# Optimization experiments

Hardware: AMD Instinct MI355X
Metric: run time of the kernel (lower is better)

The kernel has to match this reference:

```python
import jax, jax.numpy as jnp
import numpy as np

B, SX, SY, H = 4, 512, 512, 128


def setup_inputs() -> dict:
    key = jax.random.key(0)
    k1, k2, k3, k4, k5 = jax.random.split(key, 5)
    x = jax.random.normal(k1, (B, SX, 2 * H), dtype=jnp.float32)
    y = jax.random.normal(k2, (B, SY, 2 * H), dtype=jnp.float32)
    # nn.Linear(in, out, bias=False) weight has shape (out, in)
    s = 1.0 / np.sqrt(2 * H)
    Wc1 = jax.random.uniform(k3, (H, 2 * H), minval=-s, maxval=s, dtype=jnp.float32)
    Wc2 = jax.random.uniform(k4, (H, 2 * H), minval=-s, maxval=s, dtype=jnp.float32)
    sv = 1.0 / np.sqrt(H)
    vc = jax.random.uniform(k5, (1, H), minval=-sv, maxval=sv, dtype=jnp.float32)
    return {"x": x, "y": y, "Wc1": Wc1, "Wc2": Wc2, "vc": vc}


def reference(x, y, Wc1, Wc2, vc):
    # s1: (B, Sx, H), s2: (B, Sy, H)
    s1 = jnp.einsum('bsd,hd->bsh', x, Wc1)
    s2 = jnp.einsum('btd,hd->bth', y, Wc2)
    # broadcast tanh-MLP score: (B, Sy, Sx, H) -> (B, Sy, Sx)
    sjt = jnp.einsum('btsh,h->bts', jnp.tanh(s1[:, None, :, :] + s2[:, :, None, :]), vc[0])
    ait = jax.nn.softmax(sjt, axis=2)  # softmax over Sx
    qtc = jnp.einsum('bts,bsd->btd', ait, x)  # (B, Sy, 2H)
    return qtc
```

## Files before the change

kernel.cpp:

```cpp
#include <hip/hip_runtime.h>


#define NB 4
#define SEQ 512
#define HDIM 128
#define DDIM 256

static constexpr float TWO_LOG2E = 2.8853900817779268f;
static constexpr float LOG2E     = 1.4426950408889634f;

__global__ __launch_bounds__(256) void wtrans_kernel(
    const float* __restrict__ W1, const float* __restrict__ W2,
    float* __restrict__ Wt1, float* __restrict__ Wt2)
{
    __shared__ float sT[32 * 132];
    const int blk = blockIdx.x;
    const int which = blk >> 3;
    const int s = blk & 7;
    const float* W  = which ? W2 : W1;
    float*       Wt = which ? Wt2 : Wt1;
    const int tid = threadIdx.x;

    #pragma unroll
    for (int i = 0; i < 4; ++i) {
        const int idx = i * 256 + tid;
        const int h = idx >> 3, k4 = idx & 7;
        const float4 v = ((const float4*)W)[h * 64 + s * 8 + k4];
        sT[(k4 * 4 + 0) * 132 + h] = v.x;
        sT[(k4 * 4 + 1) * 132 + h] = v.y;
        sT[(k4 * 4 + 2) * 132 + h] = v.z;
        sT[(k4 * 4 + 3) * 132 + h] = v.w;
    }
    __syncthreads();
    #pragma unroll
    for (int i = 0; i < 4; ++i) {
        const int idx = i * 256 + tid;
        const int kl = idx >> 5, hq = idx & 31;
        float4 o;
        o.x = sT[kl * 132 + 4 * hq + 0];
        o.y = sT[kl * 132 + 4 * hq + 1];
        o.z = sT[kl * 132 + 4 * hq + 2];
        o.w = sT[kl * 132 + 4 * hq + 3];
        ((float4*)Wt)[(s * 32 + kl) * 32 + hq] = o;
    }
}

__global__ __launch_bounds__(256) void proj_kernel(
    const float* __restrict__ x, const float* __restrict__ y,
    const float* __restrict__ Wt1, const float* __restrict__ Wt2,
    float* __restrict__ e1sw, float* __restrict__ e2)
{
    __shared__ float As[2048];
    __shared__ float sPr[8192];
    const int tid = threadIdx.x;
    const int gr0 = blockIdx.x * 8;

    const float* in; const float* Wt; int srow;
    if (gr0 < 2048) { in = x; Wt = Wt1; srow = gr0; }
    else            { in = y; Wt = Wt2; srow = gr0 - 2048; }

    #pragma unroll
    for (int j = 0; j < 2; ++j) {
        const int idx = tid + j * 256;
        const int r = idx >> 6, kk = idx & 63;
        *(float4*)&As[idx * 4] =
            *(const float4*)&in[(srow + r) * 256 + kk * 4];
    }
    __syncthreads();

    const int hq = tid & 31;
    const int ks = tid >> 5;
    const float4* Wt4 = (const float4*)Wt;

    float4 acc4[8];
    #pragma unroll
    for (int r = 0; r < 8; ++r) acc4[r] = make_float4(0.f, 0.f, 0.f, 0.f);

    #pragma unroll
    for (int u = 0; u < 8; ++u) {
        const int kof = ks * 32 + u * 4;
        const float4 w0 = Wt4[(kof + 0) * 32 + hq];
        const float4 w1 = Wt4[(kof + 1) * 32 + hq];
        const float4 w2 = Wt4[(kof + 2) * 32 + hq];
        const float4 w3 = Wt4[(kof + 3) * 32 + hq];
        #pragma unroll
        for (int r = 0; r < 8; ++r) {
            const float4 a = *(const float4*)&As[r * 256 + kof];
            acc4[r].x = fmaf(a.w,w3.x, fmaf(a.z,w2.x, fmaf(a.y,w1.x, fmaf(a.x,w0.x, acc4[r].x))));
            acc4[r].y = fmaf(a.w,w3.y, fmaf(a.z,w2.y, fmaf(a.y,w1.y, fmaf(a.x,w0.y, acc4[r].y))));
            acc4[r].z = fmaf(a.w,w3.z, fmaf(a.z,w2.z, fmaf(a.y,w1.z, fmaf(a.x,w0.z, acc4[r].z))));
            acc4[r].w = fmaf(a.w,w3.w, fmaf(a.z,w2.w, fmaf(a.y,w1.w, fmaf(a.x,w0.w, acc4[r].w))));
        }
    }
    #pragma unroll
    for (int r = 0; r < 8; ++r)
        *(float4*)&sPr[ks * 1024 + r * 128 + hq * 4] = acc4[r];
    __syncthreads();
    {
        const int r = tid >> 5, h4 = tid & 31;
        float4 s = make_float4(0.f, 0.f, 0.f, 0.f);
        #pragma unroll
        for (int k2 = 0; k2 < 8; ++k2) {
            const float4 p = *(const float4*)&sPr[k2 * 1024 + r * 128 + h4 * 4];
            s.x += p.x; s.y += p.y; s.z += p.z; s.w += p.w;
        }
        float4 o;
        o.x = __builtin_amdgcn_exp2f(s.x * TWO_LOG2E);
        o.y = __builtin_amdgcn_exp2f(s.y * TWO_LOG2E);
        o.z = __builtin_amdgcn_exp2f(s.z * TWO_LOG2E);
        o.w = __builtin_amdgcn_exp2f(s.w * TWO_LOG2E);
        const int gr = gr0 + r;
        if (gr < 2048) {
            const int b = gr >> 9, ss = gr & 511;
            const int c = ss >> 6, sl = ss & 63;
            ((float4*)e1sw)[((b * 8 + c) * 32 + h4) * 64 + (sl ^ h4)] = o;
        } else {
            ((float4*)e2)[(gr - 2048) * 32 + h4] = o;
        }
    }
}

__global__ __launch_bounds__(1024) void score_kernel(
    const float* __restrict__ e1sw, const float* __restrict__ e2g,
    const float* __restrict__ vc,  float* __restrict__ P)
{
    __shared__ float sPartC[2][2][16 * 256];
    __shared__ float sScore[4 * 512];

    const int tid  = threadIdx.x;
    const int b    = blockIdx.x >> 7;
    const int t0   = (blockIdx.x & 127) * 4;
    const int w    = tid >> 6;
    const int lane = tid & 63;
    const int wu   = __builtin_amdgcn_readfirstlane(w);
    const int hg   = wu;

    float4 vcs[2];
    float4 e2s[4][2];
    #pragma unroll
    for (int j = 0; j < 2; ++j)
        vcs[j] = *(const float4*)&vc[(hg * 2 + j) * 4];
    #pragma unroll
    for (int t = 0; t < 4; ++t)
        #pragma unroll
        for (int j = 0; j < 2; ++j)
            e2s[t][j] = *(const float4*)&e2g[(b * SEQ + t0 + t) * HDIM + (hg * 2 + j) * 4];

    const float4* e1c = (const float4*)e1sw + b * 16384;

    const int off0 = (hg * 2 + 0) * 64 + (lane ^ (hg * 2 + 0));
    const int off1 = (hg * 2 + 1) * 64 + (lane ^ (hg * 2 + 1));

    float4 e1v0 = e1c[off0];
    float4 e1v1 = e1c[off1];

    for (int c = 0; c < 8; ++c) {
        float4 e1n0 = e1v0, e1n1 = e1v1;
        if (c < 7) {
            const float4* nx = e1c + (c + 1) * 2048;
            e1n0 = nx[off0];
            e1n1 = nx[off1];
        }
        float acc0 = 0.f, acc1 = 0.f, acc2 = 0.f, acc3 = 0.f;
        #pragma unroll
        for (int j = 0; j < 2; ++j) {
            const float4 e1 = j ? e1v1 : e1v0;
            const float4 vv = vcs[j];
            #pragma unroll
            for (int t = 0; t < 4; ++t) {
                const float4 e2 = e2s[t][j];
                const float f1 = fmaf(e1.x, e2.x, 1.f);
                const float f2 = fmaf(e1.y, e2.y, 1.f);
                const float f3 = fmaf(e1.z, e2.z, 1.f);
                const float f4 = fmaf(e1.w, e2.w, 1.f);
                const float f12 = f1 * f2, f34 = f3 * f4;
                const float n12 = fmaf(vv.x, f2, vv.y * f1);
                const float n34 = fmaf(vv.z, f4, vv.w * f3);
                const float num = fmaf(n12, f34, n34 * f12);
                const float r = fmaf(num, __builtin_amdgcn_rcpf(f12 * f34),
                                     (t == 0) ? acc0 : (t == 1) ? acc1 : (t == 2) ? acc2 : acc3);
                if      (t == 0) acc0 = r;
                else if (t == 1) acc1 = r;
                else if (t == 2) acc2 = r;
                else             acc3 = r;
            }
        }
        float* pb = &sPartC[(c >> 1) & 1][c & 1][0] + wu * 256 + lane;
        pb[0 * 64] = acc0;
        pb[1 * 64] = acc1;
        pb[2 * 64] = acc2;
        pb[3 * 64] = acc3;
        if (c & 1) {
            __syncthreads();
            if (tid < 512) {
                const int ch = tid >> 8;
                const int t  = (tid >> 6) & 3, s = tid & 63;
                const float* pc = &sPartC[(c >> 1) & 1][ch][0] + t * 64 + s;
                float r = 0.f;
                #pragma unroll
                for (int ww = 0; ww < 16; ++ww) r += pc[ww * 256];
                sScore[t * 512 + (c - 1 + ch) * 64 + s] = -2.f * r;
            }
        }
        e1v0 = e1n0;
        e1v1 = e1n1;
    }
    __syncthreads();

    if (w < 4) {
        float v[8];
        float m = -1e30f;
        #pragma unroll
        for (int j = 0; j < 8; ++j) {
            v[j] = sScore[w * 512 + lane + j * 64];
            m = fmaxf(m, v[j]);
        }
        #pragma unroll
        for (int off = 32; off; off >>= 1) m = fmaxf(m, __shfl_xor(m, off));
        float sum = 0.f;
        #pragma unroll
        for (int j = 0; j < 8; ++j) {
            v[j] = __builtin_amdgcn_exp2f((v[j] - m) * LOG2E);
            sum += v[j];
        }
        #pragma unroll
        for (int off = 32; off; off >>= 1) sum += __shfl_xor(sum, off);
        const float inv = __builtin_amdgcn_rcpf(sum);
        float* Prow = &P[(b * SEQ + t0 + w) * SEQ];
        #pragma unroll
        for (int j = 0; j < 8; ++j)
            Prow[lane + j * 64] = v[j] * inv;
    }
}

__global__ __launch_bounds__(1024) void pax_kernel(
    const float* __restrict__ P, const float* __restrict__ x,
    float* __restrict__ out)
{
    __shared__ float sP[SEQ * 8];
    __shared__ float sRed[8 * 8 * DDIM];
    const int tid = threadIdx.x;
    const int b   = blockIdx.x >> 6;
    const int t0  = (blockIdx.x & 63) * 8;
    const int w    = tid >> 6;
    const int lane = tid & 63;

    {
        const int t = tid >> 7, c4 = tid & 127;
        const float4 p = *(const float4*)&P[(b * SEQ + t0 + t) * SEQ + c4 * 4];
        sP[(c4 * 4 + 0) * 8 + t] = p.x;
        sP[(c4 * 4 + 1) * 8 + t] = p.y;
        sP[(c4 * 4 + 2) * 8 + t] = p.z;
        sP[(c4 * 4 + 3) * 8 + t] = p.w;
    }
    __syncthreads();

    const float4* x4 = (const float4*)x;
    float4 acc[8];
    #pragma unroll
    for (int t = 0; t < 8; ++t) acc[t] = make_float4(0.f, 0.f, 0.f, 0.f);

    #pragma unroll 4
    for (int si = 0; si < 32; ++si) {
        const int s = w * 32 + si;
        const float4 xv  = x4[(b * SEQ + s) * 64 + lane];
        const float4 p03 = *(const float4*)&sP[s * 8];
        const float4 p47 = *(const float4*)&sP[s * 8 + 4];
        acc[0].x = fmaf(p03.x, xv.x, acc[0].x); acc[0].y = fmaf(p03.x, xv.y, acc[0].y);
        acc[0].z = fmaf(p03.x, xv.z, acc[0].z); acc[0].w = fmaf(p03.x, xv.w, acc[0].w);
        acc[1].x = fmaf(p03.y, xv.x, acc[1].x); acc[1].y = fmaf(p03.y, xv.y, acc[1].y);
        acc[1].z = fmaf(p03.y, xv.z, acc[1].z); acc[1].w = fmaf(p03.y, xv.w, acc[1].w);
        acc[2].x = fmaf(p03.z, xv.x, acc[2].x); acc[2].y = fmaf(p03.z, xv.y, acc[2].y);
        acc[2].z = fmaf(p03.z, xv.z, acc[2].z); acc[2].w = fmaf(p03.z, xv.w, acc[2].w);
        acc[3].x = fmaf(p03.w, xv.x, acc[3].x); acc[3].y = fmaf(p03.w, xv.y, acc[3].y);
        acc[3].z = fmaf(p03.w, xv.z, acc[3].z); acc[3].w = fmaf(p03.w, xv.w, acc[3].w);
        acc[4].x = fmaf(p47.x, xv.x, acc[4].x); acc[4].y = fmaf(p47.x, xv.y, acc[4].y);
        acc[4].z = fmaf(p47.x, xv.z, acc[4].z); acc[4].w = fmaf(p47.x, xv.w, acc[4].w);
        acc[5].x = fmaf(p47.y, xv.x, acc[5].x); acc[5].y = fmaf(p47.y, xv.y, acc[5].y);
        acc[5].z = fmaf(p47.y, xv.z, acc[5].z); acc[5].w = fmaf(p47.y, xv.w, acc[5].w);
        acc[6].x = fmaf(p47.z, xv.x, acc[6].x); acc[6].y = fmaf(p47.z, xv.y, acc[6].y);
        acc[6].z = fmaf(p47.z, xv.z, acc[6].z); acc[6].w = fmaf(p47.z, xv.w, acc[6].w);
        acc[7].x = fmaf(p47.w, xv.x, acc[7].x); acc[7].y = fmaf(p47.w, xv.y, acc[7].y);
        acc[7].z = fmaf(p47.w, xv.z, acc[7].z); acc[7].w = fmaf(p47.w, xv.w, acc[7].w);
    }

    float4* sRed4 = (float4*)sRed;
    if (w < 8) {
        #pragma unroll
        for (int t = 0; t < 8; ++t)
            sRed4[w * 512 + t * 64 + lane] = acc[t];
    }
    __syncthreads();
    if (w >= 8) {
        #pragma unroll
        for (int t = 0; t < 8; ++t) {
            float4 r = sRed4[(w - 8) * 512 + t * 64 + lane];
            r.x += acc[t].x; r.y += acc[t].y; r.z += acc[t].z; r.w += acc[t].w;
            sRed4[(w - 8) * 512 + t * 64 + lane] = r;
        }
    }
    __syncthreads();
    #pragma unroll
    for (int j = 0; j < 2; ++j) {
        const int i = tid + j * 1024;
        const int t = i >> 8, d = i & 255;
        float r = 0.f;
        #pragma unroll
        for (int q = 0; q < 8; ++q) r += sRed[q * 2048 + t * 256 + d];
        out[(b * SEQ + t0 + t) * DDIM + d] = r;
    }
}

extern "C" void kernel_launch(void* const* d_in, const int* in_sizes, int n_in,
                              void* d_out, int out_size, void* d_ws, size_t ws_size,
                              hipStream_t stream) {
    const float* x   = (const float*)d_in[0];
    const float* y   = (const float*)d_in[1];
    const float* W1  = (const float*)d_in[2];
    const float* W2  = (const float*)d_in[3];
    const float* vc  = (const float*)d_in[4];
    float* outp = (float*)d_out;

    float* ws  = (float*)d_ws;
    float* e1  = ws;
    float* e2  = ws + NB * SEQ * HDIM;
    float* P   = ws + 2 * NB * SEQ * HDIM;
    float* Wt1 = P + NB * SEQ * SEQ;
    float* Wt2 = Wt1 + HDIM * DDIM;

    hipLaunchKernelGGL(wtrans_kernel, dim3(16),  dim3(256),  0, stream,
                       W1, W2, Wt1, Wt2);
    hipLaunchKernelGGL(proj_kernel,   dim3(512), dim3(256),  0, stream,
                       x, y, Wt1, Wt2, e1, e2);
    hipLaunchKernelGGL(score_kernel,  dim3(512), dim3(1024), 0, stream,
                       e1, e2, vc, P);
    hipLaunchKernelGGL(pax_kernel,    dim3(256), dim3(1024), 0, stream,
                       P, x, outp);
}
```

Before: 97.98 us.

## Fuse score/softmax kernel with P·x kernel, keeping probabilities in LDS

Merges the score+softmax kernel and the probability-times-x kernel into one launch. Each block now handles 8 query rows instead of 4, and the softmax result goes straight into shared memory instead of a global P buffer. This removes the global write and read of the 4x512x512 probability matrix and one kernel launch. In exchange the grid is halved to 256 blocks, register pressure rises from doubled e2 and accumulator state, and the score phase now syncs every chunk rather than every other chunk.

```diff
diff --git a/kernel.cpp b/kernel.cpp
--- a/kernel.cpp
+++ b/kernel.cpp
@@ -120,28 +120,28 @@
     }
 }
 
-__global__ __launch_bounds__(1024) void score_kernel(
+__global__ __launch_bounds__(1024) void score_pax_kernel(
     const float* __restrict__ e1sw, const float* __restrict__ e2g,
-    const float* __restrict__ vc,  float* __restrict__ P)
+    const float* __restrict__ vc,  const float* __restrict__ x,
+    float* __restrict__ out)
 {
-    __shared__ float sPartC[2][2][16 * 256];
-    __shared__ float sScore[4 * 512];
+    __shared__ float sBig[16384];
 
     const int tid  = threadIdx.x;
-    const int b    = blockIdx.x >> 7;
-    const int t0   = (blockIdx.x & 127) * 4;
+    const int b    = blockIdx.x >> 6;
+    const int t0   = (blockIdx.x & 63) * 8;
     const int w    = tid >> 6;
     const int lane = tid & 63;
     const int wu   = __builtin_amdgcn_readfirstlane(w);
     const int hg   = wu;
 
     float4 vcs[2];
-    float4 e2s[4][2];
+    float4 e2s[8][2];
     #pragma unroll
     for (int j = 0; j < 2; ++j)
         vcs[j] = *(const float4*)&vc[(hg * 2 + j) * 4];
     #pragma unroll
-    for (int t = 0; t < 4; ++t)
+    for (int t = 0; t < 8; ++t)
         #pragma unroll
         for (int j = 0; j < 2; ++j)
             e2s[t][j] = *(const float4*)&e2g[(b * SEQ + t0 + t) * HDIM + (hg * 2 + j) * 4];
@@ -153,6 +153,8 @@
 
     float4 e1v0 = e1c[off0];
     float4 e1v1 = e1c[off1];
+
+    float v[8];
 
     for (int c = 0; c < 8; ++c) {
         float4 e1n0 = e1v0, e1n1 = e1v1;
@@ -161,13 +163,15 @@
             e1n0 = nx[off0];
             e1n1 = nx[off1];
         }
-        float acc0 = 0.f, acc1 = 0.f, acc2 = 0.f, acc3 = 0.f;
+        float acc[8];
+        #pragma unroll
+        for (int t = 0; t < 8; ++t) acc[t] = 0.f;
         #pragma unroll
         for (int j = 0; j < 2; ++j) {
             const float4 e1 = j ? e1v1 : e1v0;
             const float4 vv = vcs[j];
             #pragma unroll
-            for (int t = 0; t < 4; ++t) {
+            for (int t = 0; t < 8; ++t) {
                 const float4 e2 = e2s[t][j];
                 const float f1 = fmaf(e1.x, e2.x, 1.f);
                 const float f2 = fmaf(e1.y, e2.y, 1.f);
@@ -177,44 +181,30 @@
                 const float n12 = fmaf(vv.x, f2, vv.y * f1);
                 const float n34 = fmaf(vv.z, f4, vv.w * f3);
                 const float num = fmaf(n12, f34, n34 * f12);
-                const float r = fmaf(num, __builtin_amdgcn_rcpf(f12 * f34),
-                                     (t == 0) ? acc0 : (t == 1) ? acc1 : (t == 2) ? acc2 : acc3);
-                if      (t == 0) acc0 = r;
-                else if (t == 1) acc1 = r;
-                else if (t == 2) acc2 = r;
-                else             acc3 = r;
+                acc[t] = fmaf(num, __builtin_amdgcn_rcpf(f12 * f34), acc[t]);
             }
         }
-        float* pb = &sPartC[(c >> 1) & 1][c & 1][0] + wu * 256 + lane;
-        pb[0 * 64] = acc0;
-        pb[1 * 64] = acc1;
-        pb[2 * 64] = acc2;
-        pb[3 * 64] = acc3;
-        if (c & 1) {
-            __syncthreads();
-            if (tid < 512) {
-                const int ch = tid >> 8;
-                const int t  = (tid >> 6) & 3, s = tid & 63;
-                const float* pc = &sPartC[(c >> 1) & 1][ch][0] + t * 64 + s;
-                float r = 0.f;
-                #pragma unroll
-                for (int ww = 0; ww < 16; ++ww) r += pc[ww * 256];
-                sScore[t * 512 + (c - 1 + ch) * 64 + s] = -2.f * r;
-            }
+        float* pb = sBig + (c & 1) * 8192 + wu * 512 + lane;
+        #pragma unroll
+        for (int t = 0; t < 8; ++t) pb[t * 64] = acc[t];
+        __syncthreads();
+        if (tid < 512) {
+            const int t = tid >> 6, s = tid & 63;
+            const float* pc = sBig + (c & 1) * 8192 + t * 64 + s;
+            float r = 0.f;
+            #pragma unroll
+            for (int ww = 0; ww < 16; ++ww) r += pc[ww * 512];
+            v[c] = -2.f * r;
         }
         e1v0 = e1n0;
         e1v1 = e1n1;
     }
-    __syncthreads();
-
-    if (w < 4) {
-        float v[8];
+
+    if (tid < 512) {
+        const int t = w;
         float m = -1e30f;
         #pragma unroll
-        for (int j = 0; j < 8; ++j) {
-            v[j] = sScore[w * 512 + lane + j * 64];
-            m = fmaxf(m, v[j]);
-        }
+        for (int j = 0; j < 8; ++j) m = fmaxf(m, v[j]);
         #pragma unroll
         for (int off = 32; off; off >>= 1) m = fmaxf(m, __shfl_xor(m, off));
         float sum = 0.f;
@@ -226,32 +216,9 @@
         #pragma unroll
         for (int off = 32; off; off >>= 1) sum += __shfl_xor(sum, off);
         const float inv = __builtin_amdgcn_rcpf(sum);
-        float* Prow = &P[(b * SEQ + t0 + w) * SEQ];
         #pragma unroll
         for (int j = 0; j < 8; ++j)
-            Prow[lane + j * 64] = v[j] * inv;
-    }
-}
-
-__global__ __launch_bounds__(1024) void pax_kernel(
-    const float* __restrict__ P, const float* __restrict__ x,
-    float* __restrict__ out)
-{
-    __shared__ float sP[SEQ * 8];
-    __shared__ float sRed[8 * 8 * DDIM];
-    const int tid = threadIdx.x;
-    const int b   = blockIdx.x >> 6;
-    const int t0  = (blockIdx.x & 63) * 8;
-    const int w    = tid >> 6;
-    const int lane = tid & 63;
-
-    {
-        const int t = tid >> 7, c4 = tid & 127;
-        const float4 p = *(const float4*)&P[(b * SEQ + t0 + t) * SEQ + c4 * 4];
-        sP[(c4 * 4 + 0) * 8 + t] = p.x;
-        sP[(c4 * 4 + 1) * 8 + t] = p.y;
-        sP[(c4 * 4 + 2) * 8 + t] = p.z;
-        sP[(c4 * 4 + 3) * 8 + t] = p.w;
+            sBig[(j * 64 + lane) * 8 + t] = v[j] * inv;
     }
     __syncthreads();
 
@@ -264,8 +231,8 @@
     for (int si = 0; si < 32; ++si) {
         const int s = w * 32 + si;
         const float4 xv  = x4[(b * SEQ + s) * 64 + lane];
-        const float4 p03 = *(const float4*)&sP[s * 8];
-        const float4 p47 = *(const float4*)&sP[s * 8 + 4];
+        const float4 p03 = *(const float4*)&sBig[s * 8];
+        const float4 p47 = *(const float4*)&sBig[s * 8 + 4];
         acc[0].x = fmaf(p03.x, xv.x, acc[0].x); acc[0].y = fmaf(p03.x, xv.y, acc[0].y);
         acc[0].z = fmaf(p03.x, xv.z, acc[0].z); acc[0].w = fmaf(p03.x, xv.w, acc[0].w);
         acc[1].x = fmaf(p03.y, xv.x, acc[1].x); acc[1].y = fmaf(p03.y, xv.y, acc[1].y);
@@ -283,8 +250,9 @@
         acc[7].x = fmaf(p47.w, xv.x, acc[7].x); acc[7].y = fmaf(p47.w, xv.y, acc[7].y);
         acc[7].z = fmaf(p47.w, xv.z, acc[7].z); acc[7].w = fmaf(p47.w, xv.w, acc[7].w);
     }
-
-    float4* sRed4 = (float4*)sRed;
+    __syncthreads();
+
+    float4* sRed4 = (float4*)sBig;
     if (w < 8) {
         #pragma unroll
         for (int t = 0; t < 8; ++t)
@@ -306,7 +274,7 @@
         const int t = i >> 8, d = i & 255;
         float r = 0.f;
         #pragma unroll
-        for (int q = 0; q < 8; ++q) r += sRed[q * 2048 + t * 256 + d];
+        for (int q = 0; q < 8; ++q) r += sBig[q * 2048 + t * 256 + d];
         out[(b * SEQ + t0 + t) * DDIM + d] = r;
     }
 }
@@ -324,16 +292,13 @@
     float* ws  = (float*)d_ws;
     float* e1  = ws;
     float* e2  = ws + NB * SEQ * HDIM;
-    float* P   = ws + 2 * NB * SEQ * HDIM;
-    float* Wt1 = P + NB * SEQ * SEQ;
+    float* Wt1 = ws + 2 * NB * SEQ * HDIM;
     float* Wt2 = Wt1 + HDIM * DDIM;
 
-    hipLaunchKernelGGL(wtrans_kernel, dim3(16),  dim3(256),  0, stream,
+    hipLaunchKernelGGL(wtrans_kernel,    dim3(16),  dim3(256),  0, stream,
                        W1, W2, Wt1, Wt2);
-    hipLaunchKernelGGL(proj_kernel,   dim3(512), dim3(256),  0, stream,
+    hipLaunchKernelGGL(proj_kernel,      dim3(512), dim3(256),  0, stream,
                        x, y, Wt1, Wt2, e1, e2);
-    hipLaunchKernelGGL(score_kernel,  dim3(512), dim3(1024), 0, stream,
-                       e1, e2, vc, P);
-    hipLaunchKernelGGL(pax_kernel,    dim3(256), dim3(1024), 0, stream,
-                       P, x, outp);
+    hipLaunchKernelGGL(score_pax_kernel, dim3(256), dim3(1024), 0, stream,
+                       e1, e2, vc, x, outp);
 }
```

Measured after the change: 95.91 us. 1.02x faster.
